# Performance work log

Measured on AMD Instinct MI355X. Metric: run time of the kernel, lower is better.

Reference implementation:

```python
import jax, jax.numpy as jnp
import numpy as np

N_SEGMENTS = 4096
D_IN = 128
D_OUT = 128
N_NODES = 1000000


def setup_inputs() -> dict:
    key = jax.random.key(0)
    ks = jax.random.split(key, 10)
    s = 1.0 / np.sqrt(D_IN)
    so = 1.0 / np.sqrt(D_OUT)
    x = jax.random.normal(ks[0], (N_NODES, D_IN), dtype=jnp.float32)
    idx = jnp.sort(jax.random.randint(ks[1], (N_NODES,), 0, N_SEGMENTS))
    return {
        "x": x,
        "idx": idx,
        "phi_w1": jax.random.uniform(ks[2], (D_IN, D_OUT), jnp.float32, -s, s),
        "phi_b1": jax.random.uniform(ks[3], (D_OUT,), jnp.float32, -s, s),
        "phi_w2": jax.random.uniform(ks[4], (D_OUT, D_OUT), jnp.float32, -so, so),
        "phi_b2": jax.random.uniform(ks[5], (D_OUT,), jnp.float32, -so, so),
        "rho_w1": jax.random.uniform(ks[6], (D_IN, D_OUT), jnp.float32, -s, s),
        "rho_b1": jax.random.uniform(ks[7], (D_OUT,), jnp.float32, -s, s),
        "rho_w2": jax.random.uniform(ks[8], (D_OUT, D_OUT), jnp.float32, -so, so),
        "rho_b2": jax.random.uniform(ks[9], (D_OUT,), jnp.float32, -so, so),
    }


def _mlp(x, w1, b1, w2, b2):
    h = jax.nn.relu(x @ w1 + b1)
    return h @ w2 + b2


def reference(x, idx, phi_w1, phi_b1, phi_w2, phi_b2, rho_w1, rho_b1, rho_w2, rho_b2):
    # phi applied per node: [N, d_out]
    x_phi = _mlp(x, phi_w1, phi_b1, phi_w2, phi_b2)
    # scatter-sum over segments: [S, d_in]
    x_sum = jax.ops.segment_sum(x, idx, num_segments=N_SEGMENTS)
    # original applies rho to the broadcasted sum; rho is a per-row MLP so
    # rho(sum)[idx] == rho(sum[idx]) -- apply once per segment, then gather.
    rho_sum = _mlp(x_sum, rho_w1, rho_b1, rho_w2, rho_b2)  # [S, d_out]
    return x_phi + rho_sum[idx]
```

## Files before the change

kernel.cpp:

```cpp
#include <hip/hip_runtime.h>
#include <hip/hip_bf16.h>

#define N_SEG 4096
#define D 128

typedef __bf16 bf16;
typedef __attribute__((ext_vector_type(8))) __bf16 bf16x8;
typedef __attribute__((ext_vector_type(4))) __bf16 bf16x4;
typedef __attribute__((ext_vector_type(4))) float floatx4;

__global__ __launch_bounds__(256) void prep_weights(
    const float* __restrict__ w1, const float* __restrict__ w2,
    bf16* __restrict__ w1t, bf16* __restrict__ w2t) {
    int i = blockIdx.x * 256 + threadIdx.x;
    int k = i >> 7, n = i & 127;
    w1t[n * 128 + k] = (bf16)w1[i];
    w2t[n * 128 + k] = (bf16)w2[i];
}

__global__ __launch_bounds__(256) void seg_sum(
    const float* __restrict__ x, const int* __restrict__ idx,
    float* __restrict__ xsum, int n) {
    int walker = threadIdx.x >> 5;
    int lane   = threadIdx.x & 31;
    long long row0 = (long long)blockIdx.x * 1024 + (long long)walker * 128;
    const float4* x4 = (const float4*)x;
    float4 acc = make_float4(0.f, 0.f, 0.f, 0.f);
    int cur = -1;
    for (int i = 0; i < 128; i++) {
        long long r = row0 + i;
        if (r >= n) break;
        int seg = idx[r];
        if (seg != cur) {
            if (cur >= 0) {
                float* p = xsum + (size_t)cur * D + lane * 4;
                atomicAdd(p + 0, acc.x); atomicAdd(p + 1, acc.y);
                atomicAdd(p + 2, acc.z); atomicAdd(p + 3, acc.w);
            }
            cur = seg;
            acc = make_float4(0.f, 0.f, 0.f, 0.f);
        }
        float4 v = x4[r * 32 + lane];
        acc.x += v.x; acc.y += v.y; acc.z += v.z; acc.w += v.w;
    }
    if (cur >= 0) {
        float* p = xsum + (size_t)cur * D + lane * 4;
        atomicAdd(p + 0, acc.x); atomicAdd(p + 1, acc.y);
        atomicAdd(p + 2, acc.z); atomicAdd(p + 3, acc.w);
    }
}

__global__ __launch_bounds__(256) void rho_mlp(
    const float* __restrict__ xsum,
    const float* __restrict__ w1, const float* __restrict__ b1,
    const float* __restrict__ w2, const float* __restrict__ b2,
    float* __restrict__ rho) {
    __shared__ float xs[8][128];
    __shared__ float hs[8][128];
    int t = threadIdx.x;
    int r0 = blockIdx.x * 8;
    for (int i = t; i < 8 * 128; i += 256) xs[i >> 7][i & 127] = xsum[(size_t)r0 * 128 + i];
    __syncthreads();
    int c = t & 127, rg = t >> 7;
    float acc[4];
#pragma unroll
    for (int p = 0; p < 4; p++) acc[p] = b1[c];
    for (int k = 0; k < 128; k++) {
        float w = w1[k * 128 + c];
#pragma unroll
        for (int p = 0; p < 4; p++) acc[p] += xs[rg * 4 + p][k] * w;
    }
#pragma unroll
    for (int p = 0; p < 4; p++) hs[rg * 4 + p][c] = fmaxf(acc[p], 0.f);
    __syncthreads();
#pragma unroll
    for (int p = 0; p < 4; p++) acc[p] = b2[c];
    for (int k = 0; k < 128; k++) {
        float w = w2[k * 128 + c];
#pragma unroll
        for (int p = 0; p < 4; p++) acc[p] += hs[rg * 4 + p][k] * w;
    }
#pragma unroll
    for (int p = 0; p < 4; p++) rho[(size_t)(r0 + rg * 4 + p) * 128 + c] = acc[p];
}

__global__ __launch_bounds__(512, 2) void phi_fused(
    const float* __restrict__ x, const int* __restrict__ idx,
    const bf16* __restrict__ w1t, const float* __restrict__ b1,
    const bf16* __restrict__ w2t, const float* __restrict__ b2,
    const float* __restrict__ rho, float* __restrict__ out, int n) {
    __shared__ bf16 xt[128][136];
    int t    = threadIdx.x;
    int wv   = t >> 6;
    int lane = t & 63;
    int m    = lane & 15;
    int q    = lane >> 4;
    long long r0 = (long long)blockIdx.x * 128;

    {
        int row = t >> 2;
        long long grow = r0 + row;
        const float4* x4 = (const float4*)x;
#pragma unroll
        for (int i = 0; i < 8; i++) {
            int c4 = (t & 3) + 4 * i;
            float4 v = make_float4(0.f, 0.f, 0.f, 0.f);
            if (grow < n) v = x4[grow * 32 + c4];
            bf16x4 pv = {(bf16)v.x, (bf16)v.y, (bf16)v.z, (bf16)v.w};
            *(bf16x4*)&xt[row][c4 * 4] = pv;
        }
    }
    const int srow0 = 16 * wv;

    floatx4 acc1[8];
#pragma unroll
    for (int nt = 0; nt < 8; nt++) acc1[nt] = (floatx4){0.f, 0.f, 0.f, 0.f};
#pragma unroll
    for (int kt = 0; kt < 4; kt++) {
        bf16x8 a = *(const bf16x8*)&xt[srow0 + m][kt * 32 + q * 8];
#pragma unroll
        for (int nt = 0; nt < 8; nt++) {
            bf16x8 b = *(const bf16x8*)&w1t[(size_t)(nt * 16 + m) * 128 + kt * 32 + q * 8];
            acc1[nt] = __builtin_amdgcn_mfma_f32_16x16x32_bf16(a, b, acc1[nt], 0, 0, 0);
        }
    }
#pragma unroll
    for (int nt = 0; nt < 8; nt++) {
        int col = nt * 16 + m;
        float bv = b1[col];
#pragma unroll
        for (int r = 0; r < 4; r++) {
            float h = fmaxf(acc1[nt][r] + bv, 0.f);
            xt[srow0 + q * 4 + r][col] = (bf16)h;
        }
    }
    floatx4 acc2[8];
#pragma unroll
    for (int nt = 0; nt < 8; nt++) acc2[nt] = (floatx4){0.f, 0.f, 0.f, 0.f};
#pragma unroll
    for (int kt = 0; kt < 4; kt++) {
        bf16x8 a = *(const bf16x8*)&xt[srow0 + m][kt * 32 + q * 8];
#pragma unroll
        for (int nt = 0; nt < 8; nt++) {
            bf16x8 b = *(const bf16x8*)&w2t[(size_t)(nt * 16 + m) * 128 + kt * 32 + q * 8];
            acc2[nt] = __builtin_amdgcn_mfma_f32_16x16x32_bf16(a, b, acc2[nt], 0, 0, 0);
        }
    }
    long long strip0 = r0 + srow0;
    long long ir = strip0 + m; if (ir > n - 1) ir = n - 1;
    int idxv = idx[ir];
    int seg[4];
#pragma unroll
    for (int r = 0; r < 4; r++) seg[r] = __shfl(idxv, q * 4 + r, 64);
#pragma unroll
    for (int nt = 0; nt < 8; nt++) {
        int col = nt * 16 + m;
        float b2v = b2[col];
#pragma unroll
        for (int r = 0; r < 4; r++) {
            long long grow = strip0 + q * 4 + r;
            if (grow < n) {
                float rv = rho[(size_t)seg[r] * 128 + col];
                out[grow * 128 + col] = acc2[nt][r] + b2v + rv;
            }
        }
    }
}

extern "C" void kernel_launch(void* const* d_in, const int* in_sizes, int n_in,
                              void* d_out, int out_size, void* d_ws, size_t ws_size,
                              hipStream_t stream) {
    const float* x      = (const float*)d_in[0];
    const int*   idx    = (const int*)d_in[1];
    const float* phi_w1 = (const float*)d_in[2];
    const float* phi_b1 = (const float*)d_in[3];
    const float* phi_w2 = (const float*)d_in[4];
    const float* phi_b2 = (const float*)d_in[5];
    const float* rho_w1 = (const float*)d_in[6];
    const float* rho_b1 = (const float*)d_in[7];
    const float* rho_w2 = (const float*)d_in[8];
    const float* rho_b2 = (const float*)d_in[9];
    float* out = (float*)d_out;
    int n = in_sizes[0] / D;

    char*  ws      = (char*)d_ws;
    float* xsum    = (float*)ws;
    float* rho_sum = (float*)(ws + (size_t)N_SEG * D * 4);
    bf16*  w1t     = (bf16*)(ws + 2 * (size_t)N_SEG * D * 4);
    bf16*  w2t     = w1t + 128 * 128;

    hipMemsetAsync(xsum, 0, (size_t)N_SEG * D * 4, stream);
    prep_weights<<<64, 256, 0, stream>>>(phi_w1, phi_w2, w1t, w2t);
    seg_sum<<<(n + 1023) / 1024, 256, 0, stream>>>(x, idx, xsum, n);
    rho_mlp<<<N_SEG / 8, 256, 0, stream>>>(xsum, rho_w1, rho_b1, rho_w2, rho_b2, rho_sum);
    phi_fused<<<(n + 127) / 128, 512, 0, stream>>>(x, idx, w1t, phi_b1, w2t, phi_b2,
                                                   rho_sum, out, n);
}
```

Baseline: 1.465 ms.

## Replace atomic segment sum with CSR bounds and per-segment block reduction

A new kernel computes segment boundaries from the sorted idx array. seg_sum then gives each segment its own block, which reduces rows with unrolled float4 loads and a shared-memory tree, so the memset and global atomics are no longer needed. The phi kernel also switches its x loads and out stores to nontemporal builtins to limit cache pollution. The cost is one extra launch, and blocks become unbalanced if segment sizes differ much.

```diff
diff --git a/kernel.cpp b/kernel.cpp
--- a/kernel.cpp
+++ b/kernel.cpp
@@ -18,35 +18,54 @@
     w2t[n * 128 + k] = (bf16)w2[i];
 }
 
+__global__ __launch_bounds__(256) void seg_bounds(
+    const int* __restrict__ idx, int* __restrict__ bounds, int n) {
+    int i = blockIdx.x * 256 + threadIdx.x;
+    if (i >= n) return;
+    int a = idx[i];
+    if (i == 0) {
+        for (int s = 0; s <= a; s++) bounds[s] = 0;
+    } else {
+        int p = idx[i - 1];
+        for (int s = p + 1; s <= a; s++) bounds[s] = i;
+    }
+    if (i == n - 1) {
+        for (int s = a + 1; s <= N_SEG; s++) bounds[s] = n;
+    }
+}
+
 __global__ __launch_bounds__(256) void seg_sum(
-    const float* __restrict__ x, const int* __restrict__ idx,
-    float* __restrict__ xsum, int n) {
-    int walker = threadIdx.x >> 5;
-    int lane   = threadIdx.x & 31;
-    long long row0 = (long long)blockIdx.x * 1024 + (long long)walker * 128;
+    const float* __restrict__ x, const int* __restrict__ bounds,
+    float* __restrict__ xsum) {
+    __shared__ float red[8][128];
+    int s = blockIdx.x;
+    int lo = bounds[s], hi = bounds[s + 1];
+    int t = threadIdx.x;
+    int c4 = t & 31, rg = t >> 5;
     const float4* x4 = (const float4*)x;
-    float4 acc = make_float4(0.f, 0.f, 0.f, 0.f);
-    int cur = -1;
-    for (int i = 0; i < 128; i++) {
-        long long r = row0 + i;
-        if (r >= n) break;
-        int seg = idx[r];
-        if (seg != cur) {
-            if (cur >= 0) {
-                float* p = xsum + (size_t)cur * D + lane * 4;
-                atomicAdd(p + 0, acc.x); atomicAdd(p + 1, acc.y);
-                atomicAdd(p + 2, acc.z); atomicAdd(p + 3, acc.w);
-            }
-            cur = seg;
-            acc = make_float4(0.f, 0.f, 0.f, 0.f);
-        }
-        float4 v = x4[r * 32 + lane];
-        acc.x += v.x; acc.y += v.y; acc.z += v.z; acc.w += v.w;
-    }
-    if (cur >= 0) {
-        float* p = xsum + (size_t)cur * D + lane * 4;
-        atomicAdd(p + 0, acc.x); atomicAdd(p + 1, acc.y);
-        atomicAdd(p + 2, acc.z); atomicAdd(p + 3, acc.w);
+    float ax = 0.f, ay = 0.f, az = 0.f, aw = 0.f;
+    int r = lo + rg;
+    for (; r + 24 < hi; r += 32) {
+        float4 v0 = x4[(size_t)(r     ) * 32 + c4];
+        float4 v1 = x4[(size_t)(r +  8) * 32 + c4];
+        float4 v2 = x4[(size_t)(r + 16) * 32 + c4];
+        float4 v3 = x4[(size_t)(r + 24) * 32 + c4];
+        ax += v0.x; ay += v0.y; az += v0.z; aw += v0.w;
+        ax += v1.x; ay += v1.y; az += v1.z; aw += v1.w;
+        ax += v2.x; ay += v2.y; az += v2.z; aw += v2.w;
+        ax += v3.x; ay += v3.y; az += v3.z; aw += v3.w;
+    }
+    for (; r < hi; r += 8) {
+        float4 v = x4[(size_t)r * 32 + c4];
+        ax += v.x; ay += v.y; az += v.z; aw += v.w;
+    }
+    *(float4*)&red[rg][c4 * 4] = make_float4(ax, ay, az, aw);
+    __syncthreads();
+    if (t < 128) {
+        float a = 0.f;
+#pragma unroll
+        for (int i = 0; i < 8; i++) a += red[i][t];
+        xsum[(size_t)s * 128 + t] = a;
     }
 }
 
@@ -100,13 +119,18 @@
     {
         int row = t >> 2;
         long long grow = r0 + row;
-        const float4* x4 = (const float4*)x;
+        const floatx4* x4 = (const floatx4*)x;
+        bool ok = grow < (long long)n;
+        floatx4 v[8];
+#pragma unroll
+        for (int i = 0; i < 8; i++) {
+            v[i] = (floatx4){0.f, 0.f, 0.f, 0.f};
+            if (ok) v[i] = __builtin_nontemporal_load(&x4[grow * 32 + (t & 3) + 4 * i]);
+        }
 #pragma unroll
         for (int i = 0; i < 8; i++) {
             int c4 = (t & 3) + 4 * i;
-            float4 v = make_float4(0.f, 0.f, 0.f, 0.f);
-            if (grow < n) v = x4[grow * 32 + c4];
-            bf16x4 pv = {(bf16)v.x, (bf16)v.y, (bf16)v.z, (bf16)v.w};
+            bf16x4 pv = {(bf16)v[i].x, (bf16)v[i].y, (bf16)v[i].z, (bf16)v[i].w};
             *(bf16x4*)&xt[row][c4 * 4] = pv;
         }
     }
@@ -161,7 +185,7 @@
             long long grow = strip0 + q * 4 + r;
             if (grow < n) {
                 float rv = rho[(size_t)seg[r] * 128 + col];
-                out[grow * 128 + col] = acc2[nt][r] + b2v + rv;
+                __builtin_nontemporal_store(acc2[nt][r] + b2v + rv, &out[grow * 128 + col]);
             }
         }
     }
@@ -188,10 +212,11 @@
     float* rho_sum = (float*)(ws + (size_t)N_SEG * D * 4);
     bf16*  w1t     = (bf16*)(ws + 2 * (size_t)N_SEG * D * 4);
     bf16*  w2t     = w1t + 128 * 128;
-
-    hipMemsetAsync(xsum, 0, (size_t)N_SEG * D * 4, stream);
+    int*   bounds  = (int*)(ws + 2 * (size_t)N_SEG * D * 4 + 2 * 128 * 128 * 2);
+
     prep_weights<<<64, 256, 0, stream>>>(phi_w1, phi_w2, w1t, w2t);
-    seg_sum<<<(n + 1023) / 1024, 256, 0, stream>>>(x, idx, xsum, n);
+    seg_bounds<<<(n + 255) / 256, 256, 0, stream>>>(idx, bounds, n);
+    seg_sum<<<N_SEG, 256, 0, stream>>>(x, bounds, xsum);
     rho_mlp<<<N_SEG / 8, 256, 0, stream>>>(xsum, rho_w1, rho_b1, rho_w2, rho_b2, rho_sum);
     phi_fused<<<(n + 127) / 128, 512, 0, stream>>>(x, idx, w1t, phi_b1, w2t, phi_b2,
                                                    rho_sum, out, n);
```

After: 1.403 ms. 4.2% less time.
